# Optimization experiments

Measured on AMD Instinct MI355X. Metric: run time of the kernel, lower is better.

Reference implementation:

```python
import jax, jax.numpy as jnp
import numpy as np

LN_EPS = 1e-5
L2_EPS = 1e-12
SCALE = 1.0 / np.sqrt(768.0)
TOPK = 8


def _ln(x, g, b):
    m = jnp.mean(x, axis=-1, keepdims=True)
    v = jnp.mean(jnp.square(x - m), axis=-1, keepdims=True)
    return (x - m) * jax.lax.rsqrt(v + LN_EPS) * g + b


def _l2norm(x):
    n = jnp.sqrt(jnp.sum(jnp.square(x), axis=-1, keepdims=True))
    return x / jnp.maximum(n, L2_EPS)


def _topk_normalize(scores, k):
    # scores: [B, K]; keep top-k, zero rest, renormalize to sum 1
    vals, idx = jax.lax.top_k(scores, k)
    B = scores.shape[0]
    weights = jnp.zeros_like(scores).at[jnp.arange(B)[:, None], idx].set(vals)
    denom = jnp.maximum(jnp.sum(weights, axis=1, keepdims=True), 1e-8)
    return weights / denom


def setup_inputs() -> dict:
    key = jax.random.key(0)
    ks = jax.random.split(key, 8)
    B, N, D, K, H, C = 32, 4096, 768, 64, 3072, 1000
    inp = {
        "patch_tokens": jax.random.normal(ks[0], (B, N, D), jnp.float32),
        "global_features": jax.random.normal(ks[1], (B, D), jnp.float32),
        "base_logits": jax.random.normal(ks[2], (B, C), jnp.float32),
        "bq": jax.random.normal(ks[3], (K, D), jnp.float32) * 0.02,
        "qn_g": jnp.ones((D,)), "qn_b": jnp.zeros((D,)),
        "tn_g": jnp.ones((D,)), "tn_b": jnp.zeros((D,)),
        "bn_g": jnp.ones((D,)), "bn_b": jnp.zeros((D,)),
        "gn_g": jnp.ones((D,)), "gn_b": jnp.zeros((D,)),
        "rln_g": jnp.ones((D,)), "rln_b": jnp.zeros((D,)),
        "rw1": jax.random.normal(ks[4], (D, H), jnp.float32) / np.sqrt(D),
        "rb1": jnp.zeros((H,)),
        "rw2": jax.random.normal(ks[5], (H, 1), jnp.float32) / np.sqrt(H),
        "rb2": jnp.zeros((1,)),
        "hw1": jax.random.normal(ks[6], (2 * D, H), jnp.float32) / np.sqrt(2 * D),
        "hb1": jnp.zeros((H,)),
        "hw2": jax.random.normal(ks[7], (H, C), jnp.float32) / np.sqrt(H),
        "hb2": jnp.zeros((C,)),
    }
    return inp


def reference(patch_tokens, global_features, base_logits, bq,
              qn_g, qn_b, tn_g, tn_b, bn_g, bn_b, gn_g, gn_b,
              rln_g, rln_b, rw1, rb1, rw2, rb2, hw1, hb1, hw2, hb2):
    # normalized cross-attention: K basis queries vs N tokens
    tokens_key = _l2norm(_ln(patch_tokens, tn_g, tn_b))           # [B,N,D]
    queries = _l2norm(_ln(bq, qn_g, qn_b))                        # [K,D]
    attn_logits = jnp.einsum('kd,bnd->bkn', queries, tokens_key) * SCALE
    attn_weights = jax.nn.softmax(attn_logits, axis=-1)           # [B,K,N]
    basis_states = jnp.einsum('bkn,bnd->bkd', attn_weights, patch_tokens)
    # routing head: LN -> Linear -> GELU -> Linear -> softplus
    r = _ln(basis_states, rln_g, rln_b)
    r = jax.nn.gelu(r @ rw1 + rb1, approximate=False)
    routing_scores = jax.nn.softplus((r @ rw2 + rb2)[..., 0])     # [B,K]
    routing_weights = _topk_normalize(routing_scores, TOPK)
    basis_summary = jnp.einsum('bk,bkd->bd', routing_weights, basis_states)
    basis_summary = _ln(basis_summary, bn_g, bn_b)
    global_summary = _ln(global_features, gn_g, gn_b)
    fused = jnp.concatenate([global_summary, basis_summary], axis=-1)
    h = jax.nn.gelu(fused @ hw1 + hb1, approximate=False)
    residual_logits = h @ hw2 + hb2
    final_logits = base_logits + residual_logits
    # diversity loss over basis queries
    bqn = _l2norm(bq)
    gram = bqn @ bqn.T
    diversity_loss = jnp.mean(jnp.square(gram - jnp.eye(gram.shape[0], dtype=gram.dtype)))
    sparse_loss = jnp.mean(routing_scores)
    return (final_logits, residual_logits, routing_weights, sparse_loss, diversity_loss)
```

## Files before the change

### kernel.cpp

```cpp
#include <hip/hip_runtime.h>
#include <math.h>

#define SCALE 0.036084391824351613f

typedef unsigned short us;
typedef __attribute__((ext_vector_type(8))) short short8;
typedef __attribute__((ext_vector_type(4))) short short4s;
typedef __attribute__((ext_vector_type(4))) float f32x4;
#define MFMA16(a, b, c) __builtin_amdgcn_mfma_f32_16x16x32_bf16(a, b, c, 0, 0, 0)

__device__ __forceinline__ us f2bf(float f) {
  unsigned u = __float_as_uint(f);
  unsigned r = (u + 0x7fffu + ((u >> 16) & 1u)) >> 16;
  return (us)r;
}
__device__ __forceinline__ float bf2f(us u) { return __uint_as_float(((unsigned)u) << 16); }

__device__ __forceinline__ void split8(f32x4 a, f32x4 b, short8& hi, short8& lo) {
  float x[8] = {a[0], a[1], a[2], a[3], b[0], b[1], b[2], b[3]};
#pragma unroll
  for (int i = 0; i < 8; i++) {
    us h = f2bf(x[i]);
    hi[i] = (short)h;
    lo[i] = (short)f2bf(x[i] - bf2f(h));
  }
}

__device__ __forceinline__ float blockReduceSum(float v, float* sh) {
#pragma unroll
  for (int o = 32; o > 0; o >>= 1) v += __shfl_xor(v, o, 64);
  int lane = threadIdx.x & 63, wid = threadIdx.x >> 6;
  __syncthreads();
  if (lane == 0) sh[wid] = v;
  __syncthreads();
  float r = sh[0];
  int nw = blockDim.x >> 6;
  for (int i = 1; i < nw; i++) r += sh[i];
  return r;
}

__device__ __forceinline__ float gelu_exact(float x) {
  return 0.5f * x * (1.0f + erff(x * 0.7071067811865476f));
}

__global__ void __launch_bounds__(256) k_prep_queries(
    const float* __restrict__ bq, const float* __restrict__ qn_g, const float* __restrict__ qn_b,
    const float* __restrict__ tn_g, const float* __restrict__ tn_b,
    us* __restrict__ qgh, us* __restrict__ qgl,
    float* __restrict__ s1, float* __restrict__ qb,
    float* __restrict__ bqn, float* __restrict__ gcons) {
  __shared__ float sh[8];
  int k = blockIdx.x, t = threadIdx.x;
  const float* xr = bq + (size_t)k * 768;
  float x0 = xr[t], x1 = xr[t + 256], x2 = xr[t + 512];
  float sx = blockReduceSum(x0 + x1 + x2, sh);
  float sxx = blockReduceSum(x0 * x0 + x1 * x1 + x2 * x2, sh);
  float mean = sx * (1.0f / 768.0f);
  float var = fmaxf(sxx * (1.0f / 768.0f) - mean * mean, 0.0f);
  float rs = rsqrtf(var + 1e-5f);
  float y0 = (x0 - mean) * rs * qn_g[t] + qn_b[t];
  float y1 = (x1 - mean) * rs * qn_g[t + 256] + qn_b[t + 256];
  float y2 = (x2 - mean) * rs * qn_g[t + 512] + qn_b[t + 512];
  float ss = blockReduceSum(y0 * y0 + y1 * y1 + y2 * y2, sh);
  float inv = 1.0f / fmaxf(sqrtf(ss), 1e-12f);
  float q0 = y0 * inv, q1 = y1 * inv, q2 = y2 * inv;
  float tg0 = tn_g[t], tg1 = tn_g[t + 256], tg2 = tn_g[t + 512];
  float tb0 = tn_b[t], tb1 = tn_b[t + 256], tb2 = tn_b[t + 512];
  float g0 = q0 * tg0, g1 = q1 * tg1, g2 = q2 * tg2;
  us h0 = f2bf(g0), h1 = f2bf(g1), h2 = f2bf(g2);
  qgh[(size_t)k * 768 + t] = h0;
  qgh[(size_t)k * 768 + t + 256] = h1;
  qgh[(size_t)k * 768 + t + 512] = h2;
  qgl[(size_t)k * 768 + t] = f2bf(g0 - bf2f(h0));
  qgl[(size_t)k * 768 + t + 256] = f2bf(g1 - bf2f(h1));
  qgl[(size_t)k * 768 + t + 512] = f2bf(g2 - bf2f(h2));
  float s1p = blockReduceSum(g0 + g1 + g2, sh);
  float qbp = blockReduceSum(q0 * tb0 + q1 * tb1 + q2 * tb2, sh);
  if (t == 0) { s1[k] = s1p; qb[k] = qbp; }
  float inv2 = 1.0f / fmaxf(sqrtf(sxx), 1e-12f);
  bqn[(size_t)k * 768 + t] = x0 * inv2;
  bqn[(size_t)k * 768 + t + 256] = x1 * inv2;
  bqn[(size_t)k * 768 + t + 512] = x2 * inv2;
  float sggp = blockReduceSum(tg0 * tg0 + tg1 * tg1 + tg2 * tg2, sh);
  float sgbp = blockReduceSum(tg0 * tb0 + tg1 * tb1 + tg2 * tb2, sh);
  float sbbp = blockReduceSum(tb0 * tb0 + tb1 * tb1 + tb2 * tb2, sh);
  if (k == 0 && t == 0) { gcons[0] = sggp; gcons[1] = sgbp; gcons[2] = sbbp; }
}

__global__ void __launch_bounds__(256) k_gram(const float* __restrict__ bqn,
                                              float* __restrict__ gpart) {
  __shared__ float bk[768];
  __shared__ float arr[64];
  int k = blockIdx.x, t = threadIdx.x;
  bk[t] = bqn[(size_t)k * 768 + t];
  bk[t + 256] = bqn[(size_t)k * 768 + t + 256];
  bk[t + 512] = bqn[(size_t)k * 768 + t + 512];
  __syncthreads();
  int j = t >> 2, sub = t & 3;
  const float* bj = bqn + (size_t)j * 768 + sub * 192;
  float v = 0.0f;
  for (int d = 0; d < 192; d++) v += bk[sub * 192 + d] * bj[d];
  v += __shfl_xor(v, 1, 64);
  v += __shfl_xor(v, 2, 64);
  if (sub == 0) { float e = v - (j == k ? 1.0f : 0.0f); arr[j] = e * e; }
  __syncthreads();
  if (t < 64) {
    float s = arr[t];
#pragma unroll
    for (int o = 32; o > 0; o >>= 1) s += __shfl_xor(s, o, 64);
    if (t == 0) gpart[k] = s;
  }
}

__global__ void __launch_bounds__(256) k_w1t(const float* __restrict__ rw1,
                                             us* __restrict__ w1th, us* __restrict__ w1tl) {
  __shared__ float tl[32][33];
  int d0 = blockIdx.x * 32, h0 = blockIdx.y * 32;
  int t = threadIdx.x, tx = t & 31, ty = t >> 5;
#pragma unroll
  for (int j = 0; j < 4; j++)
    tl[ty + j * 8][tx] = rw1[(size_t)(d0 + ty + j * 8) * 3072 + h0 + tx];
  __syncthreads();
#pragma unroll
  for (int j = 0; j < 4; j++) {
    float v = tl[tx][ty + j * 8];
    us h = f2bf(v);
    w1th[(size_t)(h0 + ty + j * 8) * 768 + d0 + tx] = h;
    w1tl[(size_t)(h0 + ty + j * 8) * 768 + d0 + tx] = f2bf(v - bf2f(h));
  }
}

__global__ void __launch_bounds__(256) k_attn_mfma(
    const float* __restrict__ x, const us* __restrict__ qgh, const us* __restrict__ qgl,
    const float* __restrict__ s1v, const float* __restrict__ qbv,
    const float* __restrict__ tng, const float* __restrict__ tnb,
    const float* __restrict__ gcons, float* __restrict__ E, float* __restrict__ rowsum) {
  __shared__ __align__(16) us qsh[64 * 32], qsl[64 * 32];
  __shared__ __align__(16) us xsh[128 * 32], xsl[128 * 32];
  __shared__ float sA[128], sB[128], sC[128];
  __shared__ float sRow[4][64];
  const int b = blockIdx.y, n0 = blockIdx.x * 128;
  const int t = threadIdx.x, w = t >> 6, l = t & 63;
  const int sr = t >> 2, sq = t & 3;
  const us* qsrcH = qgh + (size_t)sr * 768 + sq * 8;
  const us* qsrcL = qgl + (size_t)sr * 768 + sq * 8;
  const float* xsrc = x + ((size_t)b * 4096 + n0 + sr) * 768 + sq * 8;
  f32x4 acc[4][2];
#pragma unroll
  for (int i = 0; i < 4; i++)
#pragma unroll
    for (int j = 0; j < 2; j++) acc[i][j] = (f32x4){0.f, 0.f, 0.f, 0.f};
  float s0x = 0, s0xx = 0, s0a = 0, s0b = 0, s0c = 0;
  float t1x = 0, t1xx = 0, t1a = 0, t1b = 0, t1c = 0;
  short8 qh = *(const short8*)qsrcH, ql = *(const short8*)qsrcL;
  f32x4 x0a = *(const f32x4*)xsrc, x0b = *(const f32x4*)(xsrc + 4);
  f32x4 x1a = *(const f32x4*)(xsrc + (size_t)64 * 768);
  f32x4 x1b = *(const f32x4*)(xsrc + (size_t)64 * 768 + 4);
  for (int dk = 0; dk < 768; dk += 32) {
    f32x4 ga = *(const f32x4*)(tng + dk + sq * 8);
    f32x4 gA = *(const f32x4*)(tng + dk + sq * 8 + 4);
    f32x4 ba = *(const f32x4*)(tnb + dk + sq * 8);
    f32x4 bA = *(const f32x4*)(tnb + dk + sq * 8 + 4);
#pragma unroll
    for (int i = 0; i < 4; i++) {
      float g1 = ga[i], g2 = gA[i], b1 = ba[i], b2 = bA[i];
      float xv = x0a[i]; float gx = g1 * xv;
      s0x += xv; s0xx = fmaf(xv, xv, s0xx);
      s0a = fmaf(gx, gx, s0a); s0b = fmaf(g1, gx, s0b); s0c = fmaf(b1, gx, s0c);
      xv = x0b[i]; gx = g2 * xv;
      s0x += xv; s0xx = fmaf(xv, xv, s0xx);
      s0a = fmaf(gx, gx, s0a); s0b = fmaf(g2, gx, s0b); s0c = fmaf(b2, gx, s0c);
      xv = x1a[i]; gx = g1 * xv;
      t1x += xv; t1xx = fmaf(xv, xv, t1xx);
      t1a = fmaf(gx, gx, t1a); t1b = fmaf(g1, gx, t1b); t1c = fmaf(b1, gx, t1c);
      xv = x1b[i]; gx = g2 * xv;
      t1x += xv; t1xx = fmaf(xv, xv, t1xx);
      t1a = fmaf(gx, gx, t1a); t1b = fmaf(g2, gx, t1b); t1c = fmaf(b2, gx, t1c);
    }
    short8 hi, lo;
    __syncthreads();
    *(short8*)&qsh[sr * 32 + sq * 8] = qh; *(short8*)&qsl[sr * 32 + sq * 8] = ql;
    split8(x0a, x0b, hi, lo);
    *(short8*)&xsh[sr * 32 + sq * 8] = hi; *(short8*)&xsl[sr * 32 + sq * 8] = lo;
    split8(x1a, x1b, hi, lo);
    *(short8*)&xsh[(sr + 64) * 32 + sq * 8] = hi; *(short8*)&xsl[(sr + 64) * 32 + sq * 8] = lo;
    __syncthreads();
    if (dk + 32 < 768) {
      int d2 = dk + 32;
      qh = *(const short8*)(qsrcH + d2); ql = *(const short8*)(qsrcL + d2);
      x0a = *(const f32x4*)(xsrc + d2); x0b = *(const f32x4*)(xsrc + d2 + 4);
      x1a = *(const f32x4*)(xsrc + (size_t)64 * 768 + d2);
      x1b = *(const f32x4*)(xsrc + (size_t)64 * 768 + d2 + 4);
    }
    short8 ah[4], al[4];
#pragma unroll
    for (int kt = 0; kt < 4; kt++) {
      int off = (kt * 16 + (l & 15)) * 32 + (l >> 4) * 8;
      ah[kt] = *(const short8*)&qsh[off];
      al[kt] = *(const short8*)&qsl[off];
    }
#pragma unroll
    for (int nt = 0; nt < 2; nt++) {
      int off = (w * 32 + nt * 16 + (l & 15)) * 32 + (l >> 4) * 8;
      short8 bh = *(const short8*)&xsh[off];
      short8 bl = *(const short8*)&xsl[off];
#pragma unroll
      for (int kt = 0; kt < 4; kt++) {
        acc[kt][nt] = MFMA16(ah[kt], bh, acc[kt][nt]);
        acc[kt][nt] = MFMA16(ah[kt], bl, acc[kt][nt]);
        acc[kt][nt] = MFMA16(al[kt], bh, acc[kt][nt]);
        acc[kt][nt] = MFMA16(al[kt], bl, acc[kt][nt]);
      }
    }
  }
  float sgg = gcons[0], sgb = gcons[1], sbb = gcons[2];
#define R4(v) v += __shfl_xor(v, 1, 64); v += __shfl_xor(v, 2, 64)
  R4(s0x); R4(s0xx); R4(s0a); R4(s0b); R4(s0c);
  R4(t1x); R4(t1xx); R4(t1a); R4(t1b); R4(t1c);
#undef R4
  if (sq == 0) {
    {
      float m = s0x * (1.0f / 768.0f);
      float var = fmaxf(s0xx * (1.0f / 768.0f) - m * m, 0.0f);
      float rs = rsqrtf(var + 1e-5f);
      float ss = fmaxf(rs * rs * (s0a - 2.0f * m * s0b + m * m * sgg) +
                       2.0f * rs * (s0c - m * sgb) + sbb, 0.0f);
      float inv = 1.0f / fmaxf(sqrtf(ss), 1e-12f);
      float A = SCALE * inv * rs;
      sA[sr] = A; sB[sr] = A * m; sC[sr] = SCALE * inv;
    }
    {
      float m = t1x * (1.0f / 768.0f);
      float var = fmaxf(t1xx * (1.0f / 768.0f) - m * m, 0.0f);
      float rs = rsqrtf(var + 1e-5f);
      float ss = fmaxf(rs * rs * (t1a - 2.0f * m * t1b + m * m * sgg) +
                       2.0f * rs * (t1c - m * sgb) + sbb, 0.0f);
      float inv = 1.0f / fmaxf(sqrtf(ss), 1e-12f);
      float A = SCALE * inv * rs;
      sA[sr + 64] = A; sB[sr + 64] = A * m; sC[sr + 64] = SCALE * inv;
    }
  }
  __syncthreads();
  float esum[4][4];
#pragma unroll
  for (int kt = 0; kt < 4; kt++)
#pragma unroll
    for (int r = 0; r < 4; r++) esum[kt][r] = 0.f;
#pragma unroll
  for (int nt = 0; nt < 2; nt++) {
    int nn = w * 32 + nt * 16 + (l & 15);
    int n = n0 + nn;
    float Av = sA[nn], Bv = sB[nn], Cv = sC[nn];
#pragma unroll
    for (int kt = 0; kt < 4; kt++) {
#pragma unroll
      for (int r = 0; r < 4; r++) {
        int k = kt * 16 + (l >> 4) * 4 + r;
        float v = Av * acc[kt][nt][r] - Bv * s1v[k] + Cv * qbv[k];
        float e = expf(v);
        E[((size_t)b * 64 + k) * 4096 + n] = e;
        esum[kt][r] += e;
      }
    }
  }
#pragma unroll
  for (int kt = 0; kt < 4; kt++)
#pragma unroll
    for (int r = 0; r < 4; r++) {
      float e = esum[kt][r];
      e += __shfl_xor(e, 1, 64);
      e += __shfl_xor(e, 2, 64);
      e += __shfl_xor(e, 4, 64);
      e += __shfl_xor(e, 8, 64);
      if ((l & 15) == 0) sRow[w][kt * 16 + (l >> 4) * 4 + r] = e;
    }
  __syncthreads();
  if (t < 64)
    atomicAdd(&rowsum[b * 64 + t], sRow[0][t] + sRow[1][t] + sRow[2][t] + sRow[3][t]);
}

__global__ void __launch_bounds__(256) k_zero(float* __restrict__ p) {
  ((f32x4*)p)[blockIdx.x * 256 + threadIdx.x] = (f32x4){0.f, 0.f, 0.f, 0.f};
}

__global__ void __launch_bounds__(256) k_pv_mfma(
    const float* __restrict__ x, const float* __restrict__ E,
    const float* __restrict__ rowsum, float* __restrict__ S) {
  __shared__ __align__(16) us wth[64 * 32], wtl[64 * 32];
  __shared__ __align__(16) us xth[8 * 32 * 16], xtl[8 * 32 * 16];
  const int b = blockIdx.y, d0 = blockIdx.x * 128, nb = blockIdx.z * 512;
  const int t = threadIdx.x, w = t >> 6, l = t & 63;
  const int krow = t >> 2;
  const float* wsrc = E + ((size_t)b * 64 + krow) * 4096 + nb + (t & 3) * 8;
  const float ir = 1.0f / rowsum[b * 64 + krow];
  const int gg = t >> 6, nn = (t >> 1) & 31, hh = t & 1;
  const float* xsrc0 = x + ((size_t)b * 4096 + nb + nn) * 768 + d0 + gg * 16 + hh * 8;
  const float* xsrc1 = xsrc0 + 64;
  f32x4 acc[4][2];
#pragma unroll
  for (int i = 0; i < 4; i++)
#pragma unroll
    for (int j = 0; j < 2; j++) acc[i][j] = (f32x4){0.f, 0.f, 0.f, 0.f};
  f32x4 w0a = *(const f32x4*)wsrc, w0b = *(const f32x4*)(wsrc + 4);
  f32x4 xa0 = *(const f32x4*)xsrc0, xb0 = *(const f32x4*)(xsrc0 + 4);
  f32x4 xa1 = *(const f32x4*)xsrc1, xb1 = *(const f32x4*)(xsrc1 + 4);
  for (int ns = 0; ns < 512; ns += 32) {
    short8 hi, lo;
    f32x4 e0, e1;
#pragma unroll
    for (int i = 0; i < 4; i++) {
      e0[i] = w0a[i] * ir;
      e1[i] = w0b[i] * ir;
    }
    __syncthreads();
    split8(e0, e1, hi, lo);
    *(short8*)&wth[krow * 32 + (t & 3) * 8] = hi;
    *(short8*)&wtl[krow * 32 + (t & 3) * 8] = lo;
    split8(xa0, xb0, hi, lo);
    *(short8*)&xth[(size_t)t * 8] = hi; *(short8*)&xtl[(size_t)t * 8] = lo;
    split8(xa1, xb1, hi, lo);
    *(short8*)&xth[((size_t)t + 256) * 8] = hi; *(short8*)&xtl[((size_t)t + 256) * 8] = lo;
    __syncthreads();
    if (ns + 32 < 512) {
      w0a = *(const f32x4*)(wsrc + ns + 32); w0b = *(const f32x4*)(wsrc + ns + 36);
      const float* p0 = xsrc0 + (size_t)(ns + 32) * 768;
      xa0 = *(const f32x4*)p0; xb0 = *(const f32x4*)(p0 + 4);
      xa1 = *(const f32x4*)(p0 + 64); xb1 = *(const f32x4*)(p0 + 68);
    }
    short8 ah[4], al[4];
#pragma unroll
    for (int kt = 0; kt < 4; kt++) {
      int off = (kt * 16 + (l & 15)) * 32 + (l >> 4) * 8;
      ah[kt] = *(const short8*)&wth[off];
      al[kt] = *(const short8*)&wtl[off];
    }
#pragma unroll
    for (int dt = 0; dt < 2; dt++) {
      const us* gph = &xth[(2 * w + dt) * 512];
      const us* gpl = &xtl[(2 * w + dt) * 512];
      int rb = (l >> 4) * 8, cc = l & 15;
      short8 bh, bl;
#pragma unroll
      for (int i = 0; i < 8; i++) {
        bh[i] = (short)gph[(rb + i) * 16 + cc];
        bl[i] = (short)gpl[(rb + i) * 16 + cc];
      }
#pragma unroll
      for (int kt = 0; kt < 4; kt++) {
        acc[kt][dt] = MFMA16(ah[kt], bh, acc[kt][dt]);
        acc[kt][dt] = MFMA16(ah[kt], bl, acc[kt][dt]);
        acc[kt][dt] = MFMA16(al[kt], bh, acc[kt][dt]);
        acc[kt][dt] = MFMA16(al[kt], bl, acc[kt][dt]);
      }
    }
  }
#pragma unroll
  for (int dt = 0; dt < 2; dt++) {
    int d = d0 + w * 32 + dt * 16 + (l & 15);
#pragma unroll
    for (int kt = 0; kt < 4; kt++) {
#pragma unroll
      for (int r = 0; r < 4; r++) {
        int k = kt * 16 + (l >> 4) * 4 + r;
        atomicAdd(&S[((size_t)b * 64 + k) * 768 + d], acc[kt][dt][r]);
      }
    }
  }
}

__global__ void __launch_bounds__(256) k_ln768(
    const float* __restrict__ in, const float* __restrict__ g, const float* __restrict__ b,
    us* __restrict__ outh, us* __restrict__ outl) {
  int wid = threadIdx.x >> 6, lane = threadIdx.x & 63;
  size_t row = (size_t)blockIdx.x * 4 + wid;
  const f32x4* xr = (const f32x4*)(in + row * 768);
  f32x4 v[3];
  float sx = 0, sxx = 0;
#pragma unroll
  for (int j = 0; j < 3; j++) {
    v[j] = xr[lane + j * 64];
#pragma unroll
    for (int i = 0; i < 4; i++) { sx += v[j][i]; sxx = fmaf(v[j][i], v[j][i], sxx); }
  }
#pragma unroll
  for (int o = 32; o > 0; o >>= 1) { sx += __shfl_xor(sx, o, 64); sxx += __shfl_xor(sxx, o, 64); }
  float mean = sx * (1.0f / 768.0f);
  float var = fmaxf(sxx * (1.0f / 768.0f) - mean * mean, 0.0f);
  float rs = rsqrtf(var + 1e-5f);
  const f32x4* gp = (const f32x4*)g;
  const f32x4* bp = (const f32x4*)b;
#pragma unroll
  for (int j = 0; j < 3; j++) {
    f32x4 gv = gp[lane + j * 64], bv = bp[lane + j * 64];
    short4s h4, l4;
#pragma unroll
    for (int i = 0; i < 4; i++) {
      float y = (v[j][i] - mean) * rs * gv[i] + bv[i];
      us h = f2bf(y);
      h4[i] = (short)h;
      l4[i] = (short)f2bf(y - bf2f(h));
    }
    int e = (lane + j * 64) * 4;
    *(short4s*)&outh[row * 768 + e] = h4;
    *(short4s*)&outl[row * 768 + e] = l4;
  }
}

__global__ void __launch_bounds__(512) k_rh_mfma(
    const us* __restrict__ rhh, const us* __restrict__ rhl,
    const us* __restrict__ w1th, const us* __restrict__ w1tl,
    const float* __restrict__ rb1, const float* __restrict__ rw2,
    float* __restrict__ scores_raw) {
  __shared__ __align__(16) us ash[128 * 32], asl[128 * 32];
  __shared__ __align__(16) us bsh[128 * 32], bsl[128 * 32];
  __shared__ float spart[4][128];
  const int h0 = blockIdx.x * 128, m0 = blockIdx.y * 128;
  const int t = threadIdx.x, w = t >> 6, l = t & 63;
  const int wm = w >> 2, wh = w & 3;
  const int sr = t >> 2, sq = t & 3;
  const us* aH = rhh + (size_t)(m0 + sr) * 768 + sq * 8;
  const us* aL = rhl + (size_t)(m0 + sr) * 768 + sq * 8;
  const us* bH = w1th + (size_t)(h0 + sr) * 768 + sq * 8;
  const us* bL = w1tl + (size_t)(h0 + sr) * 768 + sq * 8;
  f32x4 acc[4][2];
#pragma unroll
  for (int i = 0; i < 4; i++)
#pragma unroll
    for (int j = 0; j < 2; j++) acc[i][j] = (f32x4){0.f, 0.f, 0.f, 0.f};
  short8 a0h = *(const short8*)aH, a0l = *(const short8*)aL;
  short8 b0h = *(const short8*)bH, b0l = *(const short8*)bL;
  for (int dk = 0; dk < 768; dk += 32) {
    __syncthreads();
    *(short8*)&ash[sr * 32 + sq * 8] = a0h; *(short8*)&asl[sr * 32 + sq * 8] = a0l;
    *(short8*)&bsh[sr * 32 + sq * 8] = b0h; *(short8*)&bsl[sr * 32 + sq * 8] = b0l;
    __syncthreads();
    if (dk + 32 < 768) {
      int d2 = dk + 32;
      a0h = *(const short8*)(aH + d2); a0l = *(const short8*)(aL + d2);
      b0h = *(const short8*)(bH + d2); b0l = *(const short8*)(bL + d2);
    }
    short8 ah[4], al[4];
#pragma unroll
    for (int kt = 0; kt < 4; kt++) {
      int off = ((wm * 64 + kt * 16 + (l & 15))) * 32 + (l >> 4) * 8;
      ah[kt] = *(const short8*)&ash[off];
      al[kt] = *(const short8*)&asl[off];
    }
#pragma unroll
    for (int nt = 0; nt < 2; nt++) {
      int off = ((wh * 32 + nt * 16 + (l & 15))) * 32 + (l >> 4) * 8;
      short8 bh = *(const short8*)&bsh[off];
      short8 bl = *(const short8*)&bsl[off];
#pragma unroll
      for (int kt = 0; kt < 4; kt++) {
        acc[kt][nt] = MFMA16(ah[kt], bh, acc[kt][nt]);
        acc[kt][nt] = MFMA16(ah[kt], bl, acc[kt][nt]);
        acc[kt][nt] = MFMA16(al[kt], bh, acc[kt][nt]);
        acc[kt][nt] = MFMA16(al[kt], bl, acc[kt][nt]);
      }
    }
  }
  float psum[4][4];
#pragma unroll
  for (int kt = 0; kt < 4; kt++)
#pragma unroll
    for (int r = 0; r < 4; r++) psum[kt][r] = 0.f;
#pragma unroll
  for (int nt = 0; nt < 2; nt++) {
    int h = h0 + wh * 32 + nt * 16 + (l & 15);
    float bias = rb1[h];
    float rw2v = rw2[h];
#pragma unroll
    for (int kt = 0; kt < 4; kt++) {
#pragma unroll
      for (int r = 0; r < 4; r++) {
        float g = gelu_exact(acc[kt][nt][r] + bias);
        psum[kt][r] = fmaf(g, rw2v, psum[kt][r]);
      }
    }
  }
#pragma unroll
  for (int kt = 0; kt < 4; kt++)
#pragma unroll
    for (int r = 0; r < 4; r++) {
      float v = psum[kt][r];
      v += __shfl_xor(v, 1, 64);
      v += __shfl_xor(v, 2, 64);
      v += __shfl_xor(v, 4, 64);
      v += __shfl_xor(v, 8, 64);
      if ((l & 15) == 0) spart[wh][wm * 64 + kt * 16 + (l >> 4) * 4 + r] = v;
    }
  __syncthreads();
  if (t < 128)
    atomicAdd(&scores_raw[m0 + t], spart[0][t] + spart[1][t] + spart[2][t] + spart[3][t]);
}

__global__ void __launch_bounds__(256) k_fused(
    const float* __restrict__ bs, const float* __restrict__ scores_raw,
    const float* __restrict__ rb2, const float* __restrict__ gf,
    const float* __restrict__ bn_g, const float* __restrict__ bn_b,
    const float* __restrict__ gn_g, const float* __restrict__ gn_b,
    float* __restrict__ fused, float* __restrict__ rw_out) {
  __shared__ float sh[8];
  __shared__ float wsh[64];
  int b = blockIdx.x, t = threadIdx.x;
  if (t < 64) {
    float z = scores_raw[b * 64 + t] + rb2[0];
    float s = fmaxf(z, 0.0f) + log1pf(expf(-fabsf(z)));
    bool sel = false;
    for (int it = 0; it < 8; it++) {
      float v = sel ? -INFINITY : s;
      int idx = t;
#pragma unroll
      for (int o = 32; o > 0; o >>= 1) {
        float v2 = __shfl_xor(v, o, 64);
        int i2 = __shfl_xor(idx, o, 64);
        if (v2 > v || (v2 == v && i2 < idx)) { v = v2; idx = i2; }
      }
      if (t == idx) sel = true;
    }
    float wv = sel ? s : 0.0f;
    float tot = wv;
#pragma unroll
    for (int o = 32; o > 0; o >>= 1) tot += __shfl_xor(tot, o, 64);
    float wt = wv / fmaxf(tot, 1e-8f);
    wsh[t] = wt;
    rw_out[b * 64 + t] = wt;
  }
  __syncthreads();
  float v0 = 0, v1 = 0, v2 = 0;
  const float* bsb = bs + (size_t)b * 64 * 768;
  for (int k = 0; k < 64; k++) {
    float w = wsh[k];
    if (w != 0.0f) {
      v0 = fmaf(w, bsb[(size_t)k * 768 + t], v0);
      v1 = fmaf(w, bsb[(size_t)k * 768 + t + 256], v1);
      v2 = fmaf(w, bsb[(size_t)k * 768 + t + 512], v2);
    }
  }
  float sx = blockReduceSum(v0 + v1 + v2, sh);
  float sxx = blockReduceSum(v0 * v0 + v1 * v1 + v2 * v2, sh);
  float mean = sx * (1.0f / 768.0f);
  float var = fmaxf(sxx * (1.0f / 768.0f) - mean * mean, 0.0f);
  float rs = rsqrtf(var + 1e-5f);
  float* fb = fused + (size_t)b * 1536;
  fb[768 + t] = (v0 - mean) * rs * bn_g[t] + bn_b[t];
  fb[768 + t + 256] = (v1 - mean) * rs * bn_g[t + 256] + bn_b[t + 256];
  fb[768 + t + 512] = (v2 - mean) * rs * bn_g[t + 512] + bn_b[t + 512];
  const float* gr = gf + (size_t)b * 768;
  float g0 = gr[t], g1 = gr[t + 256], g2 = gr[t + 512];
  float gsx = blockReduceSum(g0 + g1 + g2, sh);
  float gsxx = blockReduceSum(g0 * g0 + g1 * g1 + g2 * g2, sh);
  float gm = gsx * (1.0f / 768.0f);
  float gv = fmaxf(gsxx * (1.0f / 768.0f) - gm * gm, 0.0f);
  float grs = rsqrtf(gv + 1e-5f);
  fb[t] = (g0 - gm) * grs * gn_g[t] + gn_b[t];
  fb[t + 256] = (g1 - gm) * grs * gn_g[t + 256] + gn_b[t + 256];
  fb[t + 512] = (g2 - gm) * grs * gn_g[t + 512] + gn_b[t + 512];
}

__global__ void __launch_bounds__(256) k_head1(
    const float* __restrict__ fused, const float* __restrict__ hw1, const float* __restrict__ hb1,
    float* __restrict__ h) {
  __shared__ float fl[4][1536];
  __shared__ float part[4][4][64];
  int bp = blockIdx.y * 4, h0 = blockIdx.x * 64, t = threadIdx.x;
  for (int i = t; i < 1536; i += 256) {
#pragma unroll
    for (int j = 0; j < 4; j++) fl[j][i] = fused[(size_t)(bp + j) * 1536 + i];
  }
  __syncthreads();
  int c = t & 63, sl = t >> 6;
  int hh = h0 + c;
  int kbase = sl * 384;
  const float* wp = hw1 + (size_t)kbase * 3072 + hh;
  float a0 = 0.f, a1 = 0.f, a2 = 0.f, a3 = 0.f;
#pragma unroll 8
  for (int k = 0; k < 384; k++) {
    float w = wp[(size_t)k * 3072];
    a0 = fmaf(fl[0][kbase + k], w, a0);
    a1 = fmaf(fl[1][kbase + k], w, a1);
    a2 = fmaf(fl[2][kbase + k], w, a2);
    a3 = fmaf(fl[3][kbase + k], w, a3);
  }
  part[0][sl][c] = a0; part[1][sl][c] = a1; part[2][sl][c] = a2; part[3][sl][c] = a3;
  __syncthreads();
  if (sl == 0) {
    float bias = hb1[hh];
#pragma unroll
    for (int j = 0; j < 4; j++) {
      float s = part[j][0][c] + part[j][1][c] + part[j][2][c] + part[j][3][c];
      h[(size_t)(bp + j) * 3072 + hh] = gelu_exact(s + bias);
    }
  }
}

__global__ void __launch_bounds__(256) k_head2(
    const float* __restrict__ h, const float* __restrict__ hw2, const float* __restrict__ hb2,
    const float* __restrict__ base, float* __restrict__ out) {
  __shared__ float hl[2][3072];
  __shared__ float part[2][4][64];
  int bp = blockIdx.y * 2, c0 = blockIdx.x * 64, t = threadIdx.x;
  for (int i = t; i < 3072; i += 256) {
    hl[0][i] = h[(size_t)bp * 3072 + i];
    hl[1][i] = h[(size_t)(bp + 1) * 3072 + i];
  }
  __syncthreads();
  int c = t & 63, sl = t >> 6;
  int cc = c0 + c;
  int csafe = cc < 1000 ? cc : 999;
  int kbase = sl * 768;
  const float* wp = hw2 + (size_t)kbase * 1000 + csafe;
  float a0 = 0.f, a1 = 0.f;
#pragma unroll 8
  for (int k = 0; k < 768; k++) {
    float w = wp[(size_t)k * 1000];
    a0 = fmaf(hl[0][kbase + k], w, a0);
    a1 = fmaf(hl[1][kbase + k], w, a1);
  }
  part[0][sl][c] = a0; part[1][sl][c] = a1;
  __syncthreads();
  if (sl == 0 && cc < 1000) {
    float bias = hb2[cc];
    float s0 = part[0][0][c] + part[0][1][c] + part[0][2][c] + part[0][3][c] + bias;
    float s1_ = part[1][0][c] + part[1][1][c] + part[1][2][c] + part[1][3][c] + bias;
    out[32000 + bp * 1000 + cc] = s0;
    out[bp * 1000 + cc] = base[bp * 1000 + cc] + s0;
    out[32000 + (bp + 1) * 1000 + cc] = s1_;
    out[(bp + 1) * 1000 + cc] = base[(bp + 1) * 1000 + cc] + s1_;
  }
}

__global__ void __launch_bounds__(256) k_losses(
    const float* __restrict__ scores_raw, const float* __restrict__ rb2,
    const float* __restrict__ gpart, float* __restrict__ out) {
  __shared__ float sh[8];
  int t = threadIdx.x;
  float s = 0.0f;
#pragma unroll
  for (int i = 0; i < 8; i++) {
    float z = scores_raw[t + i * 256] + rb2[0];
    s += fmaxf(z, 0.0f) + log1pf(expf(-fabsf(z)));
  }
  s = blockReduceSum(s, sh);
  float gsum = (t < 64) ? gpart[t] : 0.0f;
  gsum = blockReduceSum(gsum, sh);
  if (t == 0) {
    out[66048] = s * (1.0f / 2048.0f);
    out[66049] = gsum * (1.0f / 4096.0f);
  }
}

extern "C" void kernel_launch(void* const* d_in, const int* in_sizes, int n_in,
                              void* d_out, int out_size, void* d_ws, size_t ws_size,
                              hipStream_t stream) {
  const float* patch = (const float*)d_in[0];
  const float* gfeat = (const float*)d_in[1];
  const float* base  = (const float*)d_in[2];
  const float* bq    = (const float*)d_in[3];
  const float* qn_g  = (const float*)d_in[4];
  const float* qn_b  = (const float*)d_in[5];
  const float* tn_g  = (const float*)d_in[6];
  const float* tn_b  = (const float*)d_in[7];
  const float* bn_g  = (const float*)d_in[8];
  const float* bn_b  = (const float*)d_in[9];
  const float* gn_g  = (const float*)d_in[10];
  const float* gn_b  = (const float*)d_in[11];
  const float* rln_g = (const float*)d_in[12];
  const float* rln_b = (const float*)d_in[13];
  const float* rw1   = (const float*)d_in[14];
  const float* rb1   = (const float*)d_in[15];
  const float* rw2   = (const float*)d_in[16];
  const float* rb2   = (const float*)d_in[17];
  const float* hw1   = (const float*)d_in[18];
  const float* hb1   = (const float*)d_in[19];
  const float* hw2   = (const float*)d_in[20];
  const float* hb2   = (const float*)d_in[21];
  float* ws = (float*)d_ws;
  float* out = (float*)d_out;

  float* s1      = ws + 0;
  float* qb      = ws + 64;
  float* gcons   = ws + 128;
  float* gpart   = ws + 160;
  float* fusedb  = ws + 224;
  float* hbuf    = ws + 49376;
  float* bqn     = ws + 147680;
  us*    qgh     = (us*)(ws + 196832);
  us*    qgl     = (us*)(ws + 221408);
  us*    w1th    = (us*)(ws + 245984);
  us*    w1tl    = (us*)(ws + 1425632);
  us*    rhh     = (us*)(ws + 2605280);
  us*    rhl     = (us*)(ws + 3391712);
  float* bs      = ws + 4178144;
  float* scores  = ws + 5751008;
  float* rowsum  = ws + 5753056;
  float* E       = ws + 5755104;

  k_prep_queries<<<dim3(64), 256, 0, stream>>>(bq, qn_g, qn_b, tn_g, tn_b,
                                               qgh, qgl, s1, qb, bqn, gcons);
  k_gram<<<dim3(64), 256, 0, stream>>>(bqn, gpart);
  k_w1t<<<dim3(24, 96), 256, 0, stream>>>(rw1, w1th, w1tl);
  k_zero<<<dim3(1540), 256, 0, stream>>>(bs);
  k_attn_mfma<<<dim3(32, 32), 256, 0, stream>>>(patch, qgh, qgl, s1, qb, tn_g, tn_b,
                                                gcons, E, rowsum);
  k_pv_mfma<<<dim3(6, 32, 8), 256, 0, stream>>>(patch, E, rowsum, bs);
  k_ln768<<<dim3(512), 256, 0, stream>>>(bs, rln_g, rln_b, rhh, rhl);
  k_rh_mfma<<<dim3(24, 16), 512, 0, stream>>>(rhh, rhl, w1th, w1tl, rb1, rw2, scores);
  k_fused<<<dim3(32), 256, 0, stream>>>(bs, scores, rb2, gfeat, bn_g, bn_b, gn_g, gn_b,
                                        fusedb, out + 64000);
  k_head1<<<dim3(48, 8), 256, 0, stream>>>(fusedb, hw1, hb1, hbuf);
  k_head2<<<dim3(16, 16), 256, 0, stream>>>(hbuf, hw2, hb2, base, out);
  k_losses<<<dim3(1), 256, 0, stream>>>(scores, rb2, gpart, out);
}
```

Measured before the change: 421.8 us.

## Fuse attention softmax numerator with PV product, defer row normalization

```diff
diff --git a/kernel.cpp b/kernel.cpp
--- a/kernel.cpp
+++ b/kernel.cpp
@@ -130,13 +130,15 @@
   }
 }
 
-__global__ void __launch_bounds__(256) k_attn_mfma(
+#define EPITCH 136
+__global__ void __launch_bounds__(256) k_attn_pv(
     const float* __restrict__ x, const us* __restrict__ qgh, const us* __restrict__ qgl,
     const float* __restrict__ s1v, const float* __restrict__ qbv,
     const float* __restrict__ tng, const float* __restrict__ tnb,
-    const float* __restrict__ gcons, float* __restrict__ E, float* __restrict__ rowsum) {
+    const float* __restrict__ gcons, float* __restrict__ rowsum, float* __restrict__ S) {
   __shared__ __align__(16) us qsh[64 * 32], qsl[64 * 32];
   __shared__ __align__(16) us xsh[128 * 32], xsl[128 * 32];
+  __shared__ __align__(16) us ehL[64 * EPITCH], elL[64 * EPITCH];
   __shared__ float sA[128], sB[128], sC[128];
   __shared__ float sRow[4][64];
   const int b = blockIdx.y, n0 = blockIdx.x * 128;
@@ -248,9 +250,8 @@
     for (int r = 0; r < 4; r++) esum[kt][r] = 0.f;
 #pragma unroll
   for (int nt = 0; nt < 2; nt++) {
-    int nn = w * 32 + nt * 16 + (l & 15);
-    int n = n0 + nn;
-    float Av = sA[nn], Bv = sB[nn], Cv = sC[nn];
+    int nl = w * 32 + nt * 16 + (l & 15);
+    float Av = sA[nl], Bv = sB[nl], Cv = sC[nl];
 #pragma unroll
     for (int kt = 0; kt < 4; kt++) {
 #pragma unroll
@@ -258,7 +259,9 @@
         int k = kt * 16 + (l >> 4) * 4 + r;
         float v = Av * acc[kt][nt][r] - Bv * s1v[k] + Cv * qbv[k];
         float e = expf(v);
-        E[((size_t)b * 64 + k) * 4096 + n] = e;
+        us h = f2bf(e);
+        ehL[k * EPITCH + nl] = h;
+        elL[k * EPITCH + nl] = f2bf(e - bf2f(h));
         esum[kt][r] += e;
       }
     }
@@ -277,102 +280,78 @@
   __syncthreads();
   if (t < 64)
     atomicAdd(&rowsum[b * 64 + t], sRow[0][t] + sRow[1][t] + sRow[2][t] + sRow[3][t]);
+  const int gg = t >> 6, nn = (t >> 1) & 31, hh = t & 1;
+  for (int dc = 0; dc < 6; dc++) {
+    const int dp = dc * 128;
+    f32x4 acc2[4][2];
+#pragma unroll
+    for (int i = 0; i < 4; i++)
+#pragma unroll
+      for (int j = 0; j < 2; j++) acc2[i][j] = (f32x4){0.f, 0.f, 0.f, 0.f};
+    for (int ns = 0; ns < 128; ns += 32) {
+      const float* xs0 = x + ((size_t)b * 4096 + n0 + ns + nn) * 768 + dp + gg * 16 + hh * 8;
+      f32x4 xa0 = *(const f32x4*)xs0, xb0 = *(const f32x4*)(xs0 + 4);
+      f32x4 xa1 = *(const f32x4*)(xs0 + 64), xb1 = *(const f32x4*)(xs0 + 68);
+      short8 hi, lo;
+      __syncthreads();
+      split8(xa0, xb0, hi, lo);
+      *(short8*)&xsh[(size_t)t * 8] = hi; *(short8*)&xsl[(size_t)t * 8] = lo;
+      split8(xa1, xb1, hi, lo);
+      *(short8*)&xsh[((size_t)t + 256) * 8] = hi; *(short8*)&xsl[((size_t)t + 256) * 8] = lo;
+      __syncthreads();
+      short8 ah[4], al[4];
+#pragma unroll
+      for (int kt = 0; kt < 4; kt++) {
+        int off = (kt * 16 + (l & 15)) * EPITCH + ns + (l >> 4) * 8;
+        ah[kt] = *(const short8*)&ehL[off];
+        al[kt] = *(const short8*)&elL[off];
+      }
+#pragma unroll
+      for (int dt = 0; dt < 2; dt++) {
+        const us* gph = &xsh[(2 * w + dt) * 512];
+        const us* gpl = &xsl[(2 * w + dt) * 512];
+        int rb = (l >> 4) * 8, cc = l & 15;
+        short8 bh, bl;
+#pragma unroll
+        for (int i = 0; i < 8; i++) {
+          bh[i] = (short)gph[(rb + i) * 16 + cc];
+          bl[i] = (short)gpl[(rb + i) * 16 + cc];
+        }
+#pragma unroll
+        for (int kt = 0; kt < 4; kt++) {
+          acc2[kt][dt] = MFMA16(ah[kt], bh, acc2[kt][dt]);
+          acc2[kt][dt] = MFMA16(ah[kt], bl, acc2[kt][dt]);
+          acc2[kt][dt] = MFMA16(al[kt], bh, acc2[kt][dt]);
+          acc2[kt][dt] = MFMA16(al[kt], bl, acc2[kt][dt]);
+        }
+      }
+    }
+#pragma unroll
+    for (int dt = 0; dt < 2; dt++) {
+      int d = dp + w * 32 + dt * 16 + (l & 15);
+#pragma unroll
+      for (int kt = 0; kt < 4; kt++) {
+#pragma unroll
+        for (int r = 0; r < 4; r++) {
+          int k = kt * 16 + (l >> 4) * 4 + r;
+          atomicAdd(&S[((size_t)b * 64 + k) * 768 + d], acc2[kt][dt][r]);
+        }
+      }
+    }
+  }
 }
 
 __global__ void __launch_bounds__(256) k_zero(float* __restrict__ p) {
   ((f32x4*)p)[blockIdx.x * 256 + threadIdx.x] = (f32x4){0.f, 0.f, 0.f, 0.f};
 }
 
-__global__ void __launch_bounds__(256) k_pv_mfma(
-    const float* __restrict__ x, const float* __restrict__ E,
-    const float* __restrict__ rowsum, float* __restrict__ S) {
-  __shared__ __align__(16) us wth[64 * 32], wtl[64 * 32];
-  __shared__ __align__(16) us xth[8 * 32 * 16], xtl[8 * 32 * 16];
-  const int b = blockIdx.y, d0 = blockIdx.x * 128, nb = blockIdx.z * 512;
-  const int t = threadIdx.x, w = t >> 6, l = t & 63;
-  const int krow = t >> 2;
-  const float* wsrc = E + ((size_t)b * 64 + krow) * 4096 + nb + (t & 3) * 8;
-  const float ir = 1.0f / rowsum[b * 64 + krow];
-  const int gg = t >> 6, nn = (t >> 1) & 31, hh = t & 1;
-  const float* xsrc0 = x + ((size_t)b * 4096 + nb + nn) * 768 + d0 + gg * 16 + hh * 8;
-  const float* xsrc1 = xsrc0 + 64;
-  f32x4 acc[4][2];
-#pragma unroll
-  for (int i = 0; i < 4; i++)
-#pragma unroll
-    for (int j = 0; j < 2; j++) acc[i][j] = (f32x4){0.f, 0.f, 0.f, 0.f};
-  f32x4 w0a = *(const f32x4*)wsrc, w0b = *(const f32x4*)(wsrc + 4);
-  f32x4 xa0 = *(const f32x4*)xsrc0, xb0 = *(const f32x4*)(xsrc0 + 4);
-  f32x4 xa1 = *(const f32x4*)xsrc1, xb1 = *(const f32x4*)(xsrc1 + 4);
-  for (int ns = 0; ns < 512; ns += 32) {
-    short8 hi, lo;
-    f32x4 e0, e1;
-#pragma unroll
-    for (int i = 0; i < 4; i++) {
-      e0[i] = w0a[i] * ir;
-      e1[i] = w0b[i] * ir;
-    }
-    __syncthreads();
-    split8(e0, e1, hi, lo);
-    *(short8*)&wth[krow * 32 + (t & 3) * 8] = hi;
-    *(short8*)&wtl[krow * 32 + (t & 3) * 8] = lo;
-    split8(xa0, xb0, hi, lo);
-    *(short8*)&xth[(size_t)t * 8] = hi; *(short8*)&xtl[(size_t)t * 8] = lo;
-    split8(xa1, xb1, hi, lo);
-    *(short8*)&xth[((size_t)t + 256) * 8] = hi; *(short8*)&xtl[((size_t)t + 256) * 8] = lo;
-    __syncthreads();
-    if (ns + 32 < 512) {
-      w0a = *(const f32x4*)(wsrc + ns + 32); w0b = *(const f32x4*)(wsrc + ns + 36);
-      const float* p0 = xsrc0 + (size_t)(ns + 32) * 768;
-      xa0 = *(const f32x4*)p0; xb0 = *(const f32x4*)(p0 + 4);
-      xa1 = *(const f32x4*)(p0 + 64); xb1 = *(const f32x4*)(p0 + 68);
-    }
-    short8 ah[4], al[4];
-#pragma unroll
-    for (int kt = 0; kt < 4; kt++) {
-      int off = (kt * 16 + (l & 15)) * 32 + (l >> 4) * 8;
-      ah[kt] = *(const short8*)&wth[off];
-      al[kt] = *(const short8*)&wtl[off];
-    }
-#pragma unroll
-    for (int dt = 0; dt < 2; dt++) {
-      const us* gph = &xth[(2 * w + dt) * 512];
-      const us* gpl = &xtl[(2 * w + dt) * 512];
-      int rb = (l >> 4) * 8, cc = l & 15;
-      short8 bh, bl;
-#pragma unroll
-      for (int i = 0; i < 8; i++) {
-        bh[i] = (short)gph[(rb + i) * 16 + cc];
-        bl[i] = (short)gpl[(rb + i) * 16 + cc];
-      }
-#pragma unroll
-      for (int kt = 0; kt < 4; kt++) {
-        acc[kt][dt] = MFMA16(ah[kt], bh, acc[kt][dt]);
-        acc[kt][dt] = MFMA16(ah[kt], bl, acc[kt][dt]);
-        acc[kt][dt] = MFMA16(al[kt], bh, acc[kt][dt]);
-        acc[kt][dt] = MFMA16(al[kt], bl, acc[kt][dt]);
-      }
-    }
-  }
-#pragma unroll
-  for (int dt = 0; dt < 2; dt++) {
-    int d = d0 + w * 32 + dt * 16 + (l & 15);
-#pragma unroll
-    for (int kt = 0; kt < 4; kt++) {
-#pragma unroll
-      for (int r = 0; r < 4; r++) {
-        int k = kt * 16 + (l >> 4) * 4 + r;
-        atomicAdd(&S[((size_t)b * 64 + k) * 768 + d], acc[kt][dt][r]);
-      }
-    }
-  }
-}
-
 __global__ void __launch_bounds__(256) k_ln768(
-    const float* __restrict__ in, const float* __restrict__ g, const float* __restrict__ b,
+    const float* __restrict__ in, const float* __restrict__ rowsum,
+    const float* __restrict__ g, const float* __restrict__ b,
     us* __restrict__ outh, us* __restrict__ outl) {
   int wid = threadIdx.x >> 6, lane = threadIdx.x & 63;
   size_t row = (size_t)blockIdx.x * 4 + wid;
+  const float ir = 1.0f / rowsum[row];
   const f32x4* xr = (const f32x4*)(in + row * 768);
   f32x4 v[3];
   float sx = 0, sxx = 0;
@@ -380,7 +359,10 @@
   for (int j = 0; j < 3; j++) {
     v[j] = xr[lane + j * 64];
 #pragma unroll
-    for (int i = 0; i < 4; i++) { sx += v[j][i]; sxx = fmaf(v[j][i], v[j][i], sxx); }
+    for (int i = 0; i < 4; i++) {
+      v[j][i] *= ir;
+      sx += v[j][i]; sxx = fmaf(v[j][i], v[j][i], sxx);
+    }
   }
 #pragma unroll
   for (int o = 32; o > 0; o >>= 1) { sx += __shfl_xor(sx, o, 64); sxx += __shfl_xor(sxx, o, 64); }
@@ -497,7 +479,8 @@
 
 __global__ void __launch_bounds__(256) k_fused(
     const float* __restrict__ bs, const float* __restrict__ scores_raw,
-    const float* __restrict__ rb2, const float* __restrict__ gf,
+    const float* __restrict__ rowsum, const float* __restrict__ rb2,
+    const float* __restrict__ gf,
     const float* __restrict__ bn_g, const float* __restrict__ bn_b,
     const float* __restrict__ gn_g, const float* __restrict__ gn_b,
     float* __restrict__ fused, float* __restrict__ rw_out) {
@@ -524,7 +507,7 @@
 #pragma unroll
     for (int o = 32; o > 0; o >>= 1) tot += __shfl_xor(tot, o, 64);
     float wt = wv / fmaxf(tot, 1e-8f);
-    wsh[t] = wt;
+    wsh[t] = wt / rowsum[b * 64 + t];
     rw_out[b * 64 + t] = wt;
   }
   __syncthreads();
@@ -695,20 +678,18 @@
   float* bs      = ws + 4178144;
   float* scores  = ws + 5751008;
   float* rowsum  = ws + 5753056;
-  float* E       = ws + 5755104;
 
   k_prep_queries<<<dim3(64), 256, 0, stream>>>(bq, qn_g, qn_b, tn_g, tn_b,
                                                qgh, qgl, s1, qb, bqn, gcons);
   k_gram<<<dim3(64), 256, 0, stream>>>(bqn, gpart);
   k_w1t<<<dim3(24, 96), 256, 0, stream>>>(rw1, w1th, w1tl);
   k_zero<<<dim3(1540), 256, 0, stream>>>(bs);
-  k_attn_mfma<<<dim3(32, 32), 256, 0, stream>>>(patch, qgh, qgl, s1, qb, tn_g, tn_b,
-                                                gcons, E, rowsum);
-  k_pv_mfma<<<dim3(6, 32, 8), 256, 0, stream>>>(patch, E, rowsum, bs);
-  k_ln768<<<dim3(512), 256, 0, stream>>>(bs, rln_g, rln_b, rhh, rhl);
+  k_attn_pv<<<dim3(32, 32), 256, 0, stream>>>(patch, qgh, qgl, s1, qb, tn_g, tn_b,
+                                              gcons, rowsum, bs);
+  k_ln768<<<dim3(512), 256, 0, stream>>>(bs, rowsum, rln_g, rln_b, rhh, rhl);
   k_rh_mfma<<<dim3(24, 16), 512, 0, stream>>>(rhh, rhl, w1th, w1tl, rb1, rw2, scores);
-  k_fused<<<dim3(32), 256, 0, stream>>>(bs, scores, rb2, gfeat, bn_g, bn_b, gn_g, gn_b,
-                                        fusedb, out + 64000);
+  k_fused<<<dim3(32), 256, 0, stream>>>(bs, scores, rowsum, rb2, gfeat,
+                                        bn_g, bn_b, gn_g, gn_b, fusedb, out + 64000);
   k_head1<<<dim3(48, 8), 256, 0, stream>>>(fusedb, hw1, hb1, hbuf);
   k_head2<<<dim3(16, 16), 256, 0, stream>>>(hbuf, hw2, hb2, base, out);
   k_losses<<<dim3(1), 256, 0, stream>>>(scores, rb2, gpart, out);
```

Result: slower. 494.2 us (+17.2%).
